# Performance work log

Hardware: AMD Instinct MI355X
Metric: run time of the kernel (lower is better)

## Reference

```python
import jax, jax.numpy as jnp
import numpy as np

E = 1024        # embedding_dim
H = 16          # num_heads
DR = 1          # downsample_rate
INT = E // DR   # internal_dim
HD = INT // H   # head dim
B, NQ, NK = 4, 2048, 2048


def setup_inputs() -> dict:
    key = jax.random.key(0)
    ks = jax.random.split(key, 11)
    s_in = 1.0 / np.sqrt(E)
    s_int = 1.0 / np.sqrt(INT)
    return {
        "q": jax.random.normal(ks[0], (B, NQ, E), jnp.float32),
        "k": jax.random.normal(ks[1], (B, NK, E), jnp.float32),
        "v": jax.random.normal(ks[2], (B, NK, E), jnp.float32),
        "wq": jax.random.normal(ks[3], (E, INT), jnp.float32) * s_in,
        "bq": jnp.zeros((INT,), jnp.float32),
        "wk": jax.random.normal(ks[4], (E, INT), jnp.float32) * s_in,
        "bk": jnp.zeros((INT,), jnp.float32),
        "wv": jax.random.normal(ks[5], (E, INT), jnp.float32) * s_in,
        "bv": jnp.zeros((INT,), jnp.float32),
        "wo": jax.random.normal(ks[6], (INT, E), jnp.float32) * s_int,
        "bo": jnp.zeros((E,), jnp.float32),
    }


def _heads(x):
    # (B, N, INT) -> (B, H, N, HD)
    b, n, c = x.shape
    return x.reshape(b, n, H, c // H).transpose(0, 2, 1, 3)


def reference(q, k, v, wq, bq, wk, bk, wv, bv, wo, bo):
    qh = _heads(q @ wq + bq)          # (B,H,NQ,HD)
    kh = _heads(k @ wk + bk)          # (B,H,NK,HD)
    vh = _heads(v @ wv + bv)          # (B,H,NK,HD)
    scale = 1.0 / np.sqrt(HD)
    attn = jnp.einsum('bhqd,bhkd->bhqk', qh, kh) * scale  # (B,H,NQ,NK)
    attn = jax.nn.softmax(attn, axis=-1)
    out = jnp.einsum('bhqk,bhkd->bhqd', attn, vh)          # (B,H,NQ,HD)
    out = out.transpose(0, 2, 1, 3).reshape(q.shape[0], qh.shape[2], INT)
    return out @ wo + bo
```

## Files before the change

### kernel.cpp

```cpp
#include <hip/hip_runtime.h>
#include <hip/hip_bf16.h>
#include <cstdint>
#include <cstddef>

typedef __bf16 bf16_t;
typedef __bf16 bf16x8 __attribute__((ext_vector_type(8)));
typedef float f32x4 __attribute__((ext_vector_type(4)));
typedef float f32x16 __attribute__((ext_vector_type(16)));
typedef uint32_t u32;

#define EDIM 1024
#define HH 16
#define HD 64
#define NSEQ 2048
#define QSCALE 0.18033688011f

__device__ __forceinline__ void async_copy16(const bf16_t* gsrc, bf16_t* lds_dst) {
    __builtin_amdgcn_global_load_lds(
        (const __attribute__((address_space(1))) uint32_t*)gsrc,
        (__attribute__((address_space(3))) uint32_t*)lds_dst,
        16, 0, 0);
}

__global__ void cvt_f32_bf16(const float* __restrict__ in, bf16_t* __restrict__ out) {
    size_t i = ((size_t)blockIdx.x * 256 + threadIdx.x) * 8;
    float4 x = *(const float4*)(in + i);
    float4 y = *(const float4*)(in + i + 4);
    bf16x8 v = {(bf16_t)x.x, (bf16_t)x.y, (bf16_t)x.z, (bf16_t)x.w,
                (bf16_t)y.x, (bf16_t)y.y, (bf16_t)y.z, (bf16_t)y.w};
    *(bf16x8*)(out + i) = v;
}

__global__ void transpose_all(const float* __restrict__ w0, const float* __restrict__ w1,
                              const float* __restrict__ w2, const float* __restrict__ w3,
                              bf16_t* __restrict__ o0, bf16_t* __restrict__ o1,
                              bf16_t* __restrict__ o2, bf16_t* __restrict__ o3) {
    __shared__ bf16_t t[64][65];
    const float* in;
    bf16_t* out;
    switch (blockIdx.z) {
        case 0: in = w0; out = o0; break;
        case 1: in = w1; out = o1; break;
        case 2: in = w2; out = o2; break;
        default: in = w3; out = o3; break;
    }
    const int tid = threadIdx.x;
    const int kt = blockIdx.x, nt = blockIdx.y;
    #pragma unroll
    for (int i = 0; i < 16; i++) {
        int idx = i * 256 + tid;
        int r = idx >> 6, c = idx & 63;
        t[r][c] = (bf16_t)in[(size_t)(kt * 64 + r) * 1024 + nt * 64 + c];
    }
    __syncthreads();
    #pragma unroll
    for (int i = 0; i < 16; i++) {
        int idx = i * 256 + tid;
        int r = idx >> 6, c = idx & 63;
        out[(size_t)(nt * 64 + r) * 1024 + kt * 64 + c] = t[c][r];
    }
}

template <int AB, int MODE, typename OUT>
__global__ __launch_bounds__(256, 2)
void gemm_nt(const void* __restrict__ Araw, const bf16_t* __restrict__ Bt,
             const float* __restrict__ bias, OUT* __restrict__ C,
             int M, int N, int K, float oscale) {
    constexpr int BM = 128, BN = 128, BK = 64;
    __shared__ bf16_t Asm[2][BM * BK];
    __shared__ bf16_t Bsm[2][BN * BK];
    const int tid = threadIdx.x;
    const int wave = tid >> 6, lane = tid & 63;
    const int quad = lane >> 4, l15 = lane & 15;
    const int bx = blockIdx.x, by = blockIdx.y;
    const int n0 = (by & 7) * BN;
    const int m0 = ((by >> 3) * 8 + bx) * BM;
    const int wm = (wave & 1) * 64, wn = (wave >> 1) * 64;

    const int srow = tid >> 1;
    const int NT = K / BK;

    f32x4 acc[4][4] = {};

    const bf16_t* Ab = (const bf16_t*)Araw;
    const float* Af = (const float*)Araw;

    auto stage = [&](int t, int buf) {
        const int k0 = t * BK;
        #pragma unroll
        for (int i = 0; i < 4; i++) {
            int s = i * 256 + tid;
            int row = s >> 3, c = s & 7;
            int kc = c ^ (row & 7);
            if (AB) {
                async_copy16(Ab + (size_t)(m0 + row) * K + k0 + kc * 8, &Asm[buf][s * 8]);
            } else {
                const float* sp = Af + (size_t)(m0 + row) * K + k0 + kc * 8;
                float4 x = *(const float4*)sp;
                float4 y = *(const float4*)(sp + 4);
                bf16x8 vv = {(bf16_t)x.x, (bf16_t)x.y, (bf16_t)x.z, (bf16_t)x.w,
                             (bf16_t)y.x, (bf16_t)y.y, (bf16_t)y.z, (bf16_t)y.w};
                *(bf16x8*)&Asm[buf][s * 8] = vv;
            }
        }
        #pragma unroll
        for (int i = 0; i < 4; i++) {
            int s = i * 256 + tid;
            int row = s >> 3, c = s & 7;
            int kc = c ^ (row & 7);
            async_copy16(Bt + (size_t)(n0 + row) * K + k0 + kc * 8, &Bsm[buf][s * 8]);
        }
    };

    stage(0, 0);

    for (int t = 0; t < NT; t++) {
        const int buf = t & 1;
        __syncthreads();

        if (t + 1 < NT) stage(t + 1, buf ^ 1);

        bf16x8 af[2][4], bfr[2][4];
        #pragma unroll
        for (int ks = 0; ks < 2; ks++) {
            #pragma unroll
            for (int mi = 0; mi < 4; mi++) {
                int row = wm + mi * 16 + l15;
                int g = ks * 4 + quad;
                af[ks][mi] = *(const bf16x8*)&Asm[buf][row * BK + ((g ^ (row & 7)) * 8)];
            }
            #pragma unroll
            for (int ni = 0; ni < 4; ni++) {
                int row = wn + ni * 16 + l15;
                int g = ks * 4 + quad;
                bfr[ks][ni] = *(const bf16x8*)&Bsm[buf][row * BK + ((g ^ (row & 7)) * 8)];
            }
        }
        #pragma unroll
        for (int ks = 0; ks < 2; ks++)
            #pragma unroll
            for (int mi = 0; mi < 4; mi++)
                #pragma unroll
                for (int ni = 0; ni < 4; ni++)
                    acc[mi][ni] = __builtin_amdgcn_mfma_f32_16x16x32_bf16(
                        af[ks][mi], bfr[ks][ni], acc[mi][ni], 0, 0, 0);
    }

    #pragma unroll
    for (int mi = 0; mi < 4; mi++) {
        #pragma unroll
        for (int ni = 0; ni < 4; ni++) {
            #pragma unroll
            for (int r = 0; r < 4; r++) {
                int m = m0 + wm + mi * 16 + quad * 4 + r;
                int nch = n0 + wn + ni * 16 + l15;
                float v = (acc[mi][ni][r] + bias[nch]) * oscale;
                if (MODE == 2) {
                    C[(size_t)m * N + nch] = (OUT)v;
                } else {
                    int b = m >> 11, n = m & 2047;
                    int h = nch >> 6, d = nch & 63;
                    if (MODE == 0)
                        C[(((size_t)(b * HH + h)) * NSEQ + n) * HD + d] = (OUT)v;
                    else
                        C[(((size_t)(b * HH + h)) * HD + d) * NSEQ + n] = (OUT)v;
                }
            }
        }
    }
}

union PW { u32 w[4]; bf16x8 v; };

__device__ __forceinline__ u32 pack_bf16(float lo, float hi) {
    union { bf16_t h[2]; u32 u; } x;
    x.h[0] = (bf16_t)lo;
    x.h[1] = (bf16_t)hi;
    return x.u;
}

__device__ __forceinline__ void half_swap(u32& a, u32& b) {
    auto r = __builtin_amdgcn_permlane32_swap(a, b, false, false);
    a = r[0];
    b = r[1];
}

__device__ __forceinline__ void softmax_pack(const f32x16 sa, float* lp,
                                             PW& f0, PW& f1) {
    float p[16];
    #pragma unroll
    for (int r = 0; r < 16; r++) {
        p[r] = __builtin_amdgcn_exp2f(sa[r]);
        lp[r & 3] += p[r];
    }
    u32 x0 = pack_bf16(p[0],  p[1]),  x1 = pack_bf16(p[2],  p[3]);
    u32 x2 = pack_bf16(p[4],  p[5]),  x3 = pack_bf16(p[6],  p[7]);
    u32 x4 = pack_bf16(p[8],  p[9]),  x5 = pack_bf16(p[10], p[11]);
    u32 x6 = pack_bf16(p[12], p[13]), x7 = pack_bf16(p[14], p[15]);
    half_swap(x0, x2); half_swap(x1, x3);
    half_swap(x4, x6); half_swap(x5, x7);
    f0.w[0] = x0; f0.w[1] = x1; f0.w[2] = x2; f0.w[3] = x3;
    f1.w[0] = x4; f1.w[1] = x5; f1.w[2] = x6; f1.w[3] = x7;
}

__global__ __launch_bounds__(256, 2)
void attn_kernel(const bf16_t* __restrict__ Qh, const bf16_t* __restrict__ Kh,
                 const bf16_t* __restrict__ Vt, bf16_t* __restrict__ out) {
    __shared__ bf16_t Ks[2][64 * 64];
    __shared__ bf16_t Vs[2][64 * 64];
    const int tid = threadIdx.x, wave = tid >> 6, lane = tid & 63;
    const int l31 = lane & 31, hi = lane >> 5;
    const int B = blockIdx.x;
    const int qt = (B >> 3) & 15;
    const int bh = (B >> 7) * 8 + (B & 7);
    const int b = bh >> 4, h = bh & 15;

    const bf16_t* kbase = Kh + (size_t)bh * NSEQ * HD;
    const bf16_t* vbase = Vt + (size_t)bh * HD * NSEQ;

    bf16x8 qf[4];
    {
        const bf16_t* qrow =
            Qh + ((size_t)bh * NSEQ + qt * 128 + wave * 32 + l31) * HD + hi * 8;
        #pragma unroll
        for (int s = 0; s < 4; s++) qf[s] = *(const bf16x8*)(qrow + s * 16);
    }

    const bf16_t *ks0, *ks1, *vs0, *vs1;
    {
        int r0 = tid >> 3, c0 = tid & 7;
        int s1 = tid + 256;
        int r1 = s1 >> 3, c1 = s1 & 7;
        ks0 = kbase + r0 * HD + (c0 ^ (r0 & 7)) * 8;
        ks1 = kbase + r1 * HD + (c1 ^ (r1 & 7)) * 8;
        vs0 = vbase + (size_t)r0 * NSEQ + (c0 ^ (r0 & 7)) * 8;
        vs1 = vbase + (size_t)r1 * NSEQ + (c1 ^ (r1 & 7)) * 8;
    }

    async_copy16(ks0, &Ks[0][tid * 8]);
    async_copy16(ks1, &Ks[0][(tid + 256) * 8]);
    async_copy16(vs0, &Vs[0][tid * 8]);
    async_copy16(vs1, &Vs[0][(tid + 256) * 8]);

    f32x16 oacc[2] = {};
    float lp[4] = {};

    for (int t = 0; t < 32; t++) {
        const int cur = t & 1;
        __syncthreads();

        if (t < 31) {
            ks0 += 64 * HD; ks1 += 64 * HD;
            vs0 += 64;      vs1 += 64;
            async_copy16(ks0, &Ks[cur ^ 1][tid * 8]);
            async_copy16(ks1, &Ks[cur ^ 1][(tid + 256) * 8]);
            async_copy16(vs0, &Vs[cur ^ 1][tid * 8]);
            async_copy16(vs1, &Vs[cur ^ 1][(tid + 256) * 8]);
        }

        const f32x16 zero = {};
        f32x16 sacc0, sacc1;
        {
            int g = hi;
            int row0 = l31, row1 = 32 + l31;
            bf16x8 ak0 = *(const bf16x8*)&Ks[cur][row0 * 64 + ((g ^ (row0 & 7)) * 8)];
            bf16x8 ak1 = *(const bf16x8*)&Ks[cur][row1 * 64 + ((g ^ (row1 & 7)) * 8)];
            __builtin_amdgcn_s_setprio(1);
            sacc0 = __builtin_amdgcn_mfma_f32_32x32x16_bf16(ak0, qf[0], zero, 0, 0, 0);
            sacc1 = __builtin_amdgcn_mfma_f32_32x32x16_bf16(ak1, qf[0], zero, 0, 0, 0);
            __builtin_amdgcn_s_setprio(0);
        }
        #pragma unroll
        for (int s = 1; s < 4; s++) {
            int g = s * 2 + hi;
            int row0 = l31;
            int row1 = 32 + l31;
            bf16x8 ak0 = *(const bf16x8*)&Ks[cur][row0 * 64 + ((g ^ (row0 & 7)) * 8)];
            bf16x8 ak1 = *(const bf16x8*)&Ks[cur][row1 * 64 + ((g ^ (row1 & 7)) * 8)];
            __builtin_amdgcn_s_setprio(1);
            sacc0 = __builtin_amdgcn_mfma_f32_32x32x16_bf16(ak0, qf[s], sacc0, 0, 0, 0);
            sacc1 = __builtin_amdgcn_mfma_f32_32x32x16_bf16(ak1, qf[s], sacc1, 0, 0, 0);
            __builtin_amdgcn_s_setprio(0);
        }

        PW pa[4];
        softmax_pack(sacc0, lp, pa[0], pa[1]);
        softmax_pack(sacc1, lp, pa[2], pa[3]);

        #pragma unroll
        for (int dt = 0; dt < 2; dt++) {
            #pragma unroll
            for (int ks = 0; ks < 4; ks++) {
                int row = dt * 32 + l31;
                int g = ks * 2 + hi;
                bf16x8 bv = *(const bf16x8*)&Vs[cur][row * 64 + ((g ^ (row & 7)) * 8)];
                __builtin_amdgcn_s_setprio(1);
                oacc[dt] = __builtin_amdgcn_mfma_f32_32x32x16_bf16(
                    pa[ks].v, bv, oacc[dt], 0, 0, 0);
                __builtin_amdgcn_s_setprio(0);
            }
        }
    }

    float lsum = (lp[0] + lp[1]) + (lp[2] + lp[3]);
    lsum += __shfl_xor(lsum, 32, 64);
    float linv = 1.f / lsum;
    float rinv[16];
    #pragma unroll
    for (int r = 0; r < 16; r++) {
        int q = (r & 3) + 8 * (r >> 2) + 4 * hi;
        rinv[r] = __shfl(linv, q, 64);
    }

    const int n0 = qt * 128 + wave * 32;
    #pragma unroll
    for (int dt = 0; dt < 2; dt++) {
        int c = h * 64 + dt * 32 + l31;
        #pragma unroll
        for (int r = 0; r < 16; r++) {
            int q = (r & 3) + 8 * (r >> 2) + 4 * hi;
            out[((size_t)b * NSEQ + n0 + q) * EDIM + c] = (bf16_t)(oacc[dt][r] * rinv[r]);
        }
    }
}

extern "C" void kernel_launch(void* const* d_in, const int* in_sizes, int n_in,
                              void* d_out, int out_size, void* d_ws, size_t ws_size,
                              hipStream_t stream) {
    const float* q  = (const float*)d_in[0];
    const float* k  = (const float*)d_in[1];
    const float* v  = (const float*)d_in[2];
    const float* wq = (const float*)d_in[3];
    const float* bq = (const float*)d_in[4];
    const float* wk = (const float*)d_in[5];
    const float* bk = (const float*)d_in[6];
    const float* wv = (const float*)d_in[7];
    const float* bv = (const float*)d_in[8];
    const float* wo = (const float*)d_in[9];
    const float* bo = (const float*)d_in[10];
    float* out = (float*)d_out;

    char* ws = (char*)d_ws;
    bf16_t* wqt = (bf16_t*)(ws + ((size_t)0  << 20));
    bf16_t* wkt = (bf16_t*)(ws + ((size_t)2  << 20));
    bf16_t* wvt = (bf16_t*)(ws + ((size_t)4  << 20));
    bf16_t* wot = (bf16_t*)(ws + ((size_t)6  << 20));

    const bool big = ws_size >= ((size_t)90 << 20);
    size_t off = big ? ((size_t)24 << 20) : ((size_t)8 << 20);
    bf16_t* X   = (bf16_t*)(ws + ((size_t)8 << 20));
    bf16_t* Qh  = (bf16_t*)(ws + off);
    bf16_t* Kh  = (bf16_t*)(ws + off + ((size_t)16 << 20));
    bf16_t* Vt  = (bf16_t*)(ws + off + ((size_t)32 << 20));
    bf16_t* ao  = (bf16_t*)(ws + off + ((size_t)48 << 20));

    dim3 tb(256);

    transpose_all<<<dim3(16, 16, 4), tb, 0, stream>>>(wq, wk, wv, wo, wqt, wkt, wvt, wot);

    dim3 gg(8, 64);
    if (big) {
        cvt_f32_bf16<<<4096, tb, 0, stream>>>(q, X);
        gemm_nt<1, 0, bf16_t><<<gg, tb, 0, stream>>>(X, wqt, bq, Qh, 8192, 1024, 1024, QSCALE);
        cvt_f32_bf16<<<4096, tb, 0, stream>>>(k, X);
        gemm_nt<1, 0, bf16_t><<<gg, tb, 0, stream>>>(X, wkt, bk, Kh, 8192, 1024, 1024, 1.0f);
        cvt_f32_bf16<<<4096, tb, 0, stream>>>(v, X);
        gemm_nt<1, 1, bf16_t><<<gg, tb, 0, stream>>>(X, wvt, bv, Vt, 8192, 1024, 1024, 1.0f);
    } else {
        gemm_nt<0, 0, bf16_t><<<gg, tb, 0, stream>>>(q, wqt, bq, Qh, 8192, 1024, 1024, QSCALE);
        gemm_nt<0, 0, bf16_t><<<gg, tb, 0, stream>>>(k, wkt, bk, Kh, 8192, 1024, 1024, 1.0f);
        gemm_nt<0, 1, bf16_t><<<gg, tb, 0, stream>>>(v, wvt, bv, Vt, 8192, 1024, 1024, 1.0f);
    }

    attn_kernel<<<1024, tb, 0, stream>>>(Qh, Kh, Vt, ao);

    gemm_nt<1, 2, float><<<gg, tb, 0, stream>>>(ao, wot, bo, out, 8192, 1024, 1024, 1.0f);
}
```

Measured before the change: 346.3 us.

## Batch QKV projections into one kernel with register-prefetched fp32 A loads

Replaces the separate fp32-to-bf16 conversion kernels and the three projection GEMM launches with a single gemm_qkv launch that covers Q, K and V across one grid, converting fp32 activations in registers. A tiles are prefetched two steps ahead into registers and B tiles through async LDS copies, with explicit waitcnt/barrier scheduling. The output GEMM gets the same depth-2 prefetch. The aim is to remove the extra memory round trip of the conversion pass and the launch overhead, at the cost of higher register pressure and hand-tuned wait counts that are fragile if wrong.

New measurement: 346.8 us. About the same (+0.1%).

```diff
diff --git a/kernel.cpp b/kernel.cpp
--- a/kernel.cpp
+++ b/kernel.cpp
@@ -20,15 +20,6 @@
         (const __attribute__((address_space(1))) uint32_t*)gsrc,
         (__attribute__((address_space(3))) uint32_t*)lds_dst,
         16, 0, 0);
-}
-
-__global__ void cvt_f32_bf16(const float* __restrict__ in, bf16_t* __restrict__ out) {
-    size_t i = ((size_t)blockIdx.x * 256 + threadIdx.x) * 8;
-    float4 x = *(const float4*)(in + i);
-    float4 y = *(const float4*)(in + i + 4);
-    bf16x8 v = {(bf16_t)x.x, (bf16_t)x.y, (bf16_t)x.z, (bf16_t)x.w,
-                (bf16_t)y.x, (bf16_t)y.y, (bf16_t)y.z, (bf16_t)y.w};
-    *(bf16x8*)(out + i) = v;
 }
 
 __global__ void transpose_all(const float* __restrict__ w0, const float* __restrict__ w1,
@@ -61,12 +52,146 @@
     }
 }
 
-template <int AB, int MODE, typename OUT>
 __global__ __launch_bounds__(256, 2)
-void gemm_nt(const void* __restrict__ Araw, const bf16_t* __restrict__ Bt,
-             const float* __restrict__ bias, OUT* __restrict__ C,
-             int M, int N, int K, float oscale) {
-    constexpr int BM = 128, BN = 128, BK = 64;
+void gemm_qkv(const float* __restrict__ Aq, const float* __restrict__ Ak,
+              const float* __restrict__ Av,
+              const bf16_t* __restrict__ Wq, const bf16_t* __restrict__ Wk,
+              const bf16_t* __restrict__ Wv,
+              const float* __restrict__ bq, const float* __restrict__ bk,
+              const float* __restrict__ bv,
+              bf16_t* __restrict__ Qh, bf16_t* __restrict__ Kh,
+              bf16_t* __restrict__ Vt) {
+    constexpr int BM = 128, BN = 128, BK = 64, K = 1024, NT = K / BK;
+    __shared__ bf16_t Asm[2][BM * BK];
+    __shared__ bf16_t Bsm[2][BN * BK];
+    const int tid = threadIdx.x;
+    const int wave = tid >> 6, lane = tid & 63;
+    const int quad = lane >> 4, l15 = lane & 15;
+    const int bx = blockIdx.x, by = blockIdx.y;
+    const int mt = (by >> 3) * 8 + bx;
+    const int n0 = (by & 7) * BN;
+    const int wt = mt >> 6;
+    const int m0 = (mt - wt * 64) * BM;
+    const int wm = (wave & 1) * 64, wn = (wave >> 1) * 64;
+
+    const float*  A    = wt == 0 ? Aq : (wt == 1 ? Ak : Av);
+    const bf16_t* Bt   = wt == 0 ? Wq : (wt == 1 ? Wk : Wv);
+    const float*  bias = wt == 0 ? bq : (wt == 1 ? bk : bv);
+    bf16_t*       Cout = wt == 0 ? Qh : (wt == 1 ? Kh : Vt);
+    const float oscale = wt == 0 ? QSCALE : 1.0f;
+
+    f32x4 acc[4][4] = {};
+    float4 ar[8];
+
+    auto loadA = [&](int t) {
+        const int k0 = t * BK;
+        #pragma unroll
+        for (int i = 0; i < 4; i++) {
+            int s = i * 256 + tid;
+            int row = s >> 3, kc = (s & 7) ^ (row & 7);
+            const float* sp = A + (size_t)(m0 + row) * K + k0 + kc * 8;
+            ar[2 * i]     = *(const float4*)sp;
+            ar[2 * i + 1] = *(const float4*)(sp + 4);
+        }
+    };
+    auto writeA = [&](int buf) {
+        #pragma unroll
+        for (int i = 0; i < 4; i++) {
+            int s = i * 256 + tid;
+            float4 x = ar[2 * i], y = ar[2 * i + 1];
+            bf16x8 vv = {(bf16_t)x.x, (bf16_t)x.y, (bf16_t)x.z, (bf16_t)x.w,
+                         (bf16_t)y.x, (bf16_t)y.y, (bf16_t)y.z, (bf16_t)y.w};
+            *(bf16x8*)&Asm[buf][s * 8] = vv;
+        }
+    };
+    auto stageB = [&](int t, int buf) {
+        const int k0 = t * BK;
+        #pragma unroll
+        for (int i = 0; i < 4; i++) {
+            int s = i * 256 + tid;
+            int row = s >> 3, kc = (s & 7) ^ (row & 7);
+            async_copy16(Bt + (size_t)(n0 + row) * K + k0 + kc * 8, &Bsm[buf][s * 8]);
+        }
+    };
+
+    loadA(0);
+    stageB(0, 0);
+    writeA(0);
+    stageB(1, 1);
+    asm volatile("s_waitcnt vmcnt(4)" ::: "memory");
+    loadA(1);
+    asm volatile("s_waitcnt lgkmcnt(0)" ::: "memory");
+    __builtin_amdgcn_s_barrier();
+    __builtin_amdgcn_sched_barrier(0);
+
+    for (int t = 0; t < NT; ++t) {
+        const int buf = t & 1;
+        bf16x8 af[2][4], bfr[2][4];
+        #pragma unroll
+        for (int ks = 0; ks < 2; ks++) {
+            #pragma unroll
+            for (int mi = 0; mi < 4; mi++) {
+                int row = wm + mi * 16 + l15;
+                int g = ks * 4 + quad;
+                af[ks][mi] = *(const bf16x8*)&Asm[buf][row * BK + ((g ^ (row & 7)) * 8)];
+            }
+            #pragma unroll
+            for (int ni = 0; ni < 4; ni++) {
+                int row = wn + ni * 16 + l15;
+                int g = ks * 4 + quad;
+                bfr[ks][ni] = *(const bf16x8*)&Bsm[buf][row * BK + ((g ^ (row & 7)) * 8)];
+            }
+        }
+        #pragma unroll
+        for (int ks = 0; ks < 2; ks++)
+            #pragma unroll
+            for (int mi = 0; mi < 4; mi++)
+                #pragma unroll
+                for (int ni = 0; ni < 4; ni++)
+                    acc[mi][ni] = __builtin_amdgcn_mfma_f32_16x16x32_bf16(
+                        af[ks][mi], bfr[ks][ni], acc[mi][ni], 0, 0, 0);
+
+        if (t + 1 < NT) {
+            __builtin_amdgcn_s_barrier();
+            __builtin_amdgcn_sched_barrier(0);
+            writeA(buf ^ 1);
+            if (t + 2 < NT) {
+                stageB(t + 2, buf);
+                asm volatile("s_waitcnt vmcnt(4)" ::: "memory");
+                loadA(t + 2);
+            } else {
+                asm volatile("s_waitcnt vmcnt(0)" ::: "memory");
+            }
+            asm volatile("s_waitcnt lgkmcnt(0)" ::: "memory");
+            __builtin_amdgcn_s_barrier();
+            __builtin_amdgcn_sched_barrier(0);
+        }
+    }
+
+    #pragma unroll
+    for (int mi = 0; mi < 4; mi++) {
+        #pragma unroll
+        for (int ni = 0; ni < 4; ni++) {
+            #pragma unroll
+            for (int r = 0; r < 4; r++) {
+                int m = m0 + wm + mi * 16 + quad * 4 + r;
+                int nch = n0 + wn + ni * 16 + l15;
+                float v = (acc[mi][ni][r] + bias[nch]) * oscale;
+                int b = m >> 11, n = m & 2047;
+                int h = nch >> 6, d = nch & 63;
+                if (wt < 2)
+                    Cout[(((size_t)(b * HH + h)) * NSEQ + n) * HD + d] = (bf16_t)v;
+                else
+                    Cout[(((size_t)(b * HH + h)) * HD + d) * NSEQ + n] = (bf16_t)v;
+            }
+        }
+    }
+}
+
+__global__ __launch_bounds__(256, 2)
+void gemm_out(const bf16_t* __restrict__ A, const bf16_t* __restrict__ Bt,
+              const float* __restrict__ bias, float* __restrict__ C) {
+    constexpr int BM = 128, BN = 128, BK = 64, K = 1024, N = 1024, NT = K / BK;
     __shared__ bf16_t Asm[2][BM * BK];
     __shared__ bf16_t Bsm[2][BN * BK];
     const int tid = threadIdx.x;
@@ -77,49 +202,32 @@
     const int m0 = ((by >> 3) * 8 + bx) * BM;
     const int wm = (wave & 1) * 64, wn = (wave >> 1) * 64;
 
-    const int srow = tid >> 1;
-    const int NT = K / BK;
-
     f32x4 acc[4][4] = {};
-
-    const bf16_t* Ab = (const bf16_t*)Araw;
-    const float* Af = (const float*)Araw;
 
     auto stage = [&](int t, int buf) {
         const int k0 = t * BK;
         #pragma unroll
         for (int i = 0; i < 4; i++) {
             int s = i * 256 + tid;
-            int row = s >> 3, c = s & 7;
-            int kc = c ^ (row & 7);
-            if (AB) {
-                async_copy16(Ab + (size_t)(m0 + row) * K + k0 + kc * 8, &Asm[buf][s * 8]);
-            } else {
-                const float* sp = Af + (size_t)(m0 + row) * K + k0 + kc * 8;
-                float4 x = *(const float4*)sp;
-                float4 y = *(const float4*)(sp + 4);
-                bf16x8 vv = {(bf16_t)x.x, (bf16_t)x.y, (bf16_t)x.z, (bf16_t)x.w,
-                             (bf16_t)y.x, (bf16_t)y.y, (bf16_t)y.z, (bf16_t)y.w};
-                *(bf16x8*)&Asm[buf][s * 8] = vv;
-            }
+            int row = s >> 3, kc = (s & 7) ^ (row & 7);
+            async_copy16(A + (size_t)(m0 + row) * K + k0 + kc * 8, &Asm[buf][s * 8]);
         }
         #pragma unroll
         for (int i = 0; i < 4; i++) {
             int s = i * 256 + tid;
-            int row = s >> 3, c = s & 7;
-            int kc = c ^ (row & 7);
+            int row = s >> 3, kc = (s & 7) ^ (row & 7);
             async_copy16(Bt + (size_t)(n0 + row) * K + k0 + kc * 8, &Bsm[buf][s * 8]);
         }
     };
 
     stage(0, 0);
-
-    for (int t = 0; t < NT; t++) {
+    stage(1, 1);
+    asm volatile("s_waitcnt vmcnt(8)" ::: "memory");
+    __builtin_amdgcn_s_barrier();
+    __builtin_amdgcn_sched_barrier(0);
+
+    for (int t = 0; t < NT; ++t) {
         const int buf = t & 1;
-        __syncthreads();
-
-        if (t + 1 < NT) stage(t + 1, buf ^ 1);
-
         bf16x8 af[2][4], bfr[2][4];
         #pragma unroll
         for (int ks = 0; ks < 2; ks++) {
@@ -144,6 +252,20 @@
                 for (int ni = 0; ni < 4; ni++)
                     acc[mi][ni] = __builtin_amdgcn_mfma_f32_16x16x32_bf16(
                         af[ks][mi], bfr[ks][ni], acc[mi][ni], 0, 0, 0);
+
+        if (t + 1 < NT) {
+            __builtin_amdgcn_s_barrier();
+            __builtin_amdgcn_sched_barrier(0);
+            if (t + 2 < NT) {
+                stage(t + 2, buf);
+                asm volatile("s_waitcnt vmcnt(8)" ::: "memory");
+            } else {
+                asm volatile("s_waitcnt vmcnt(0)" ::: "memory");
+            }
+            asm volatile("s_waitcnt lgkmcnt(0)" ::: "memory");
+            __builtin_amdgcn_s_barrier();
+            __builtin_amdgcn_sched_barrier(0);
+        }
     }
 
     #pragma unroll
@@ -154,17 +276,7 @@
             for (int r = 0; r < 4; r++) {
                 int m = m0 + wm + mi * 16 + quad * 4 + r;
                 int nch = n0 + wn + ni * 16 + l15;
-                float v = (acc[mi][ni][r] + bias[nch]) * oscale;
-                if (MODE == 2) {
-                    C[(size_t)m * N + nch] = (OUT)v;
-                } else {
-                    int b = m >> 11, n = m & 2047;
-                    int h = nch >> 6, d = nch & 63;
-                    if (MODE == 0)
-                        C[(((size_t)(b * HH + h)) * NSEQ + n) * HD + d] = (OUT)v;
-                    else
-                        C[(((size_t)(b * HH + h)) * HD + d) * NSEQ + n] = (OUT)v;
-                }
+                C[(size_t)m * N + nch] = acc[mi][ni][r] + bias[nch];
             }
         }
     }
@@ -346,33 +458,19 @@
     bf16_t* wvt = (bf16_t*)(ws + ((size_t)4  << 20));
     bf16_t* wot = (bf16_t*)(ws + ((size_t)6  << 20));
 
-    const bool big = ws_size >= ((size_t)90 << 20);
-    size_t off = big ? ((size_t)24 << 20) : ((size_t)8 << 20);
-    bf16_t* X   = (bf16_t*)(ws + ((size_t)8 << 20));
-    bf16_t* Qh  = (bf16_t*)(ws + off);
-    bf16_t* Kh  = (bf16_t*)(ws + off + ((size_t)16 << 20));
-    bf16_t* Vt  = (bf16_t*)(ws + off + ((size_t)32 << 20));
-    bf16_t* ao  = (bf16_t*)(ws + off + ((size_t)48 << 20));
+    bf16_t* Qh  = (bf16_t*)(ws + ((size_t)8  << 20));
+    bf16_t* Kh  = (bf16_t*)(ws + ((size_t)24 << 20));
+    bf16_t* Vt  = (bf16_t*)(ws + ((size_t)40 << 20));
+    bf16_t* ao  = (bf16_t*)(ws + ((size_t)56 << 20));
 
     dim3 tb(256);
 
     transpose_all<<<dim3(16, 16, 4), tb, 0, stream>>>(wq, wk, wv, wo, wqt, wkt, wvt, wot);
 
-    dim3 gg(8, 64);
-    if (big) {
-        cvt_f32_bf16<<<4096, tb, 0, stream>>>(q, X);
-        gemm_nt<1, 0, bf16_t><<<gg, tb, 0, stream>>>(X, wqt, bq, Qh, 8192, 1024, 1024, QSCALE);
-        cvt_f32_bf16<<<4096, tb, 0, stream>>>(k, X);
-        gemm_nt<1, 0, bf16_t><<<gg, tb, 0, stream>>>(X, wkt, bk, Kh, 8192, 1024, 1024, 1.0f);
-        cvt_f32_bf16<<<4096, tb, 0, stream>>>(v, X);
-        gemm_nt<1, 1, bf16_t><<<gg, tb, 0, stream>>>(X, wvt, bv, Vt, 8192, 1024, 1024, 1.0f);
-    } else {
-        gemm_nt<0, 0, bf16_t><<<gg, tb, 0, stream>>>(q, wqt, bq, Qh, 8192, 1024, 1024, QSCALE);
-        gemm_nt<0, 0, bf16_t><<<gg, tb, 0, stream>>>(k, wkt, bk, Kh, 8192, 1024, 1024, 1.0f);
-        gemm_nt<0, 1, bf16_t><<<gg, tb, 0, stream>>>(v, wvt, bv, Vt, 8192, 1024, 1024, 1.0f);
-    }
+    gemm_qkv<<<dim3(8, 192), tb, 0, stream>>>(q, k, v, wqt, wkt, wvt,
+                                              bq, bk, bv, Qh, Kh, Vt);
 
     attn_kernel<<<1024, tb, 0, stream>>>(Qh, Kh, Vt, ao);
 
-    gemm_nt<1, 2, float><<<gg, tb, 0, stream>>>(ao, wot, bo, out, 8192, 1024, 1024, 1.0f);
-}
+    gemm_out<<<dim3(8, 64), tb, 0, stream>>>(ao, wot, bo, out);
+}
```
